# Optimization experiments

Measured on AMD Instinct MI355X. Metric: run time of the kernel, lower is better.

Reference implementation:

```python
import jax, jax.numpy as jnp
import numpy as np

B, T, E, H = 4, 2048, 512, 8
D = E // H  # head_dim = 64


def setup_inputs() -> dict:
    key = jax.random.key(0)
    ks = jax.random.split(key, 9)
    s = 1.0 / np.sqrt(E)
    inp = {
        "x": jax.random.normal(ks[0], (B, T, E), dtype=jnp.float32),
        "Wq": jax.random.normal(ks[1], (E, E), dtype=jnp.float32) * s,
        "bq": jnp.zeros((E,), dtype=jnp.float32),
        "Wk": jax.random.normal(ks[2], (E, E), dtype=jnp.float32) * s,
        "bk": jnp.zeros((E,), dtype=jnp.float32),
        "Wv": jax.random.normal(ks[3], (E, E), dtype=jnp.float32) * s,
        "bv": jnp.zeros((E,), dtype=jnp.float32),
        "Wo": jax.random.normal(ks[4], (E, E), dtype=jnp.float32) * s,
        "bo": jnp.zeros((E,), dtype=jnp.float32),
    }
    return inp


def reference(x, Wq, bq, Wk, bk, Wv, bv, Wo, bo):
    # x: (B, T, E); weights stored (in, out) so y = x @ W + b
    b, t, _ = x.shape
    q = (x @ Wq + bq).reshape(b, t, H, D).transpose(0, 2, 1, 3)  # (B,H,T,D)
    k = (x @ Wk + bk).reshape(b, t, H, D).transpose(0, 2, 1, 3)  # (B,H,T,D)
    v = (x @ Wv + bv).reshape(b, t, H, D).transpose(0, 2, 1, 3)  # (B,H,T,D)
    scores = jnp.einsum("bhqd,bhkd->bhqk", q, k) / np.sqrt(D)    # (B,H,Tq,Tk)
    # faithful to source: softmax over dim=-2 (the query axis)
    attn = jax.nn.softmax(scores, axis=-2)
    out = jnp.einsum("bhqk,bhkd->bhqd", attn, v)                  # (B,H,T,D)
    # faithful to source: reshape (B,H,T,D) -> (B,T,H*D) with NO transpose
    out = out.reshape(b, t, H * D)
    return out @ Wo + bo
```

## Files before the change

kernel.cpp:

```cpp
#include <hip/hip_runtime.h>
#include <hip/hip_bf16.h>

#define NB 4
#define NT 2048
#define NE 512
#define NH 8
#define ND 64
#define BH (NB*NH)

#define LOG2E 1.44269504088896340736f

typedef __attribute__((ext_vector_type(8))) short short8;
typedef __attribute__((ext_vector_type(4))) short short4v;
typedef __attribute__((ext_vector_type(4))) float f32x4;

typedef const __attribute__((address_space(3))) short* lds_sp;

__device__ __forceinline__ f32x4 mfma16(short8 a, short8 b, f32x4 c){
  return __builtin_amdgcn_mfma_f32_16x16x32_bf16(a, b, c, 0, 0, 0);
}
__device__ __forceinline__ short f2b(float f){
  union { float f; unsigned u; } v; v.f = f;
  unsigned r = v.u + 0x7FFFu + ((v.u >> 16) & 1u);
  return (short)(r >> 16);
}
__device__ __forceinline__ float b2f(short s){
  union { unsigned u; float f; } v; v.u = ((unsigned)(unsigned short)s) << 16; return v.f;
}
__device__ __forceinline__ unsigned pk2(float a, float b){
  union { __hip_bfloat162 h; unsigned u; } v;
  v.h = __float22bfloat162_rn(make_float2(a, b));
  return v.u;
}
__device__ __forceinline__ float fexp2(float x){
#if __has_builtin(__builtin_amdgcn_exp2f)
  return __builtin_amdgcn_exp2f(x);
#else
  return __expf(0.69314718055994530942f * x);
#endif
}
__device__ __forceinline__ void gld16(const void* g, void* l){
  __builtin_amdgcn_global_load_lds((const __attribute__((address_space(1))) void*)g,
                                   (__attribute__((address_space(3))) void*)l, 16, 0, 0);
}
__device__ __forceinline__ short4v trr(lds_sp p, int imm){
  short4v r;
  asm volatile("ds_read_b64_tr_b16 %0, %1 offset:%2" : "=v"(r) : "v"(p), "i"(imm));
  return r;
}

__global__ __launch_bounds__(256) void pack_all_k(const float* __restrict__ x, short* __restrict__ xb,
                                                  const float* __restrict__ Wq, const float* __restrict__ Wk,
                                                  const float* __restrict__ Wv, const float* __restrict__ Wo,
                                                  short* __restrict__ Wt){
  int bid = blockIdx.x;
  if (bid < 2048){
    int i = bid*256 + threadIdx.x;
    f32x4 a = ((const f32x4*)x)[2*i];
    f32x4 b = ((const f32x4*)x)[2*i+1];
    union { short8 s; unsigned u[4]; } o;
    o.u[0] = pk2(a[0], a[1]);
    o.u[1] = pk2(a[2], a[3]);
    o.u[2] = pk2(b[0], b[1]);
    o.u[3] = pk2(b[2], b[3]);
    ((short8*)xb)[i] = o.s;
  } else {
    int wb = bid - 2048;
    int z = wb >> 8;
    int rem = wb & 255;
    int j0 = (rem & 15)*32, e0 = (rem >> 4)*32;
    const float* W = z==0?Wq: z==1?Wk: z==2?Wv:Wo;
    short* out = Wt + (size_t)z*NE*NE;
    __shared__ float t[32][33];
    int tx = threadIdx.x & 31, ty = threadIdx.x >> 5;
#pragma unroll
    for (int r = 0; r < 4; ++r)
      t[ty*4+r][tx] = W[(size_t)(e0+ty*4+r)*NE + j0+tx];
    __syncthreads();
#pragma unroll
    for (int r = 0; r < 4; ++r)
      out[(size_t)(j0+ty*4+r)*NE + e0+tx] = f2b(t[tx][ty*4+r]);
  }
}

__global__ __launch_bounds__(256) void gemm_qkv_k(const short* __restrict__ xb, const short* __restrict__ Wt,
                                                  const float* __restrict__ bq, const float* __restrict__ bk,
                                                  const float* __restrict__ bv,
                                                  short* __restrict__ Q, short* __restrict__ K, short* __restrict__ V){
  int bid = blockIdx.x;
  int xcd = bid & 7;
  int j = bid >> 3;
  int n0 = (j & 3) * 128;
  int p = xcd*24 + (j >> 2);
  int z = p >> 6;
  int m0 = (p & 63) * 128;

  const short* Bm = Wt + (size_t)z*NE*NE;
  const float* bias = z==0?bq: z==1?bk:bv;
  short* out = z==0?Q: z==1?K:V;
  float scale = (z==0) ? 0.125f*LOG2E : 1.0f;

  __shared__ short As[128*64];
  __shared__ short Bs[128*64];
  int tid = threadIdx.x, lane = tid & 63, wid = tid >> 6;
  int wm = wid >> 1, wn = wid & 1;
  int sr = lane >> 3, sg = lane & 7;
  int fr = lane & 15, fg = lane >> 4;

  f32x4 acc[4][4] = {};

  for (int kt = 0; kt < 8; ++kt){
    int k0 = kt*64;
#pragma unroll
    for (int jj = 0; jj < 4; ++jj){
      int ii = wid*4 + jj;
      int r = ii*8 + sr;
      gld16(xb + (size_t)(m0 + r)*NE + k0 + ((sg ^ sr)<<3), (short*)As + ii*512);
      gld16(Bm + (size_t)(n0 + r)*NE + k0 + ((sg ^ sr)<<3), (short*)Bs + ii*512);
    }
    __syncthreads();
    short8 af[4][2], bf[4][2];
#pragma unroll
    for (int m = 0; m < 4; ++m){
      int row = wm*64 + m*16 + fr;
#pragma unroll
      for (int dh = 0; dh < 2; ++dh)
        af[m][dh] = *(const short8*)&As[row*64 + (((dh*4+fg) ^ (row&7))<<3)];
    }
#pragma unroll
    for (int n = 0; n < 4; ++n){
      int row = wn*64 + n*16 + fr;
#pragma unroll
      for (int dh = 0; dh < 2; ++dh)
        bf[n][dh] = *(const short8*)&Bs[row*64 + (((dh*4+fg) ^ (row&7))<<3)];
    }
#pragma unroll
    for (int m = 0; m < 4; ++m)
#pragma unroll
      for (int n = 0; n < 4; ++n){
        acc[m][n] = mfma16(af[m][0], bf[n][0], acc[m][n]);
        acc[m][n] = mfma16(af[m][1], bf[n][1], acc[m][n]);
      }
    __syncthreads();
  }
#pragma unroll
  for (int m = 0; m < 4; ++m)
#pragma unroll
    for (int n = 0; n < 4; ++n)
#pragma unroll
      for (int i = 0; i < 4; ++i){
        int row = m0 + wm*64 + m*16 + fg*4 + i;
        int col = n0 + wn*64 + n*16 + fr;
        float v = (acc[m][n][i] + bias[col]) * scale;
        int b = row >> 11, t = row & (NT-1), h = col >> 6, d = col & 63;
        out[(((size_t)(b*NH + h)*NT + t)<<6) + d] = f2b(v);
      }
}

__global__ __launch_bounds__(512, 4) void attn_l_k(const short* __restrict__ Q, const short* __restrict__ K,
                                                   const short* __restrict__ V, short* __restrict__ Vp){
  int bid = blockIdx.x;
  int bh = (bid & 7)*4 + ((bid >> 3) & 3);
  int kt = bid >> 5;
  const short* Qh = Q + (size_t)bh*NT*ND;
  const short* Kh = K + (size_t)bh*NT*ND;
  __shared__ short Qs0[8192];
  __shared__ short Qs1[8192];
  __shared__ float rl_all[128];
  int tid = threadIdx.x, lane = tid&63, wid = tid>>6;
  int fr = lane&15, fg = lane>>4;
  int sr = lane>>3, sg = lane&7;

  int krow = kt*128 + wid*16;
  short8 ak[2];
#pragma unroll
  for (int dh = 0; dh < 2; ++dh)
    ak[dh] = *(const short8*)&Kh[(size_t)(krow + fr)*ND + dh*32 + fg*8];

  const short* qsrc0 = Qh + (size_t)(wid*16 + sr)*ND + ((sg ^ sr)<<3);
  const short* qsrc1 = qsrc0 + 8*ND;
  auto stageQ = [&](short* qb, int t){
    size_t adv = (size_t)t*128*ND;
    gld16(qsrc0 + adv, qb + wid*1024);
    gld16(qsrc1 + adv, qb + wid*1024 + 512);
  };

  float rs[4] = {0.f,0.f,0.f,0.f};

  auto computeQ = [&](const short* Qt){
#pragma unroll
    for (int qf = 0; qf < 8; ++qf){
      int row = qf*16 + fr;
      short8 b0 = *(const short8*)&Qt[row*64 + ((fg ^ (row&7))<<3)];
      short8 b1 = *(const short8*)&Qt[row*64 + (((4+fg) ^ (row&7))<<3)];
      f32x4 c = {};
      c = mfma16(ak[0], b0, c);
      c = mfma16(ak[1], b1, c);
#pragma unroll
      for (int i = 0; i < 4; ++i)
        rs[i] += fexp2(c[i]);
    }
  };

  stageQ(Qs0, 0);
  __syncthreads();

  for (int qt2 = 0; qt2 < 8; ++qt2){
    int qtA = qt2*2;
    stageQ(Qs1, qtA+1);
    computeQ(Qs0);
    __syncthreads();
    if (qtA+2 < 16) stageQ(Qs0, qtA+2);
    computeQ(Qs1);
    __syncthreads();
  }

#pragma unroll
  for (int i = 0; i < 4; ++i){
    float v = rs[i];
    v += __shfl_xor(v, 1); v += __shfl_xor(v, 2);
    v += __shfl_xor(v, 4); v += __shfl_xor(v, 8);
    if (fr == 0) rl_all[wid*16 + fg*4 + i] = 1.0f / v;
  }
  {
    int row = tid >> 2;
    int col0 = (tid & 3) * 16;
    float inv = rl_all[row];
    const short* vsrc = V  + (size_t)bh*NT*ND + (size_t)(kt*128 + row)*ND + col0;
    short*       vdst = Vp + (size_t)bh*NT*ND + (size_t)(kt*128 + row)*ND + col0;
    short8 v0 = *(const short8*)vsrc;
    short8 v1 = *(const short8*)(vsrc + 8);
    union { short8 s; unsigned u[4]; } o0, o1;
#pragma unroll
    for (int j = 0; j < 4; ++j){
      o0.u[j] = pk2(b2f(v0[2*j])*inv, b2f(v0[2*j+1])*inv);
      o1.u[j] = pk2(b2f(v1[2*j])*inv, b2f(v1[2*j+1])*inv);
    }
    *(short8*)vdst       = o0.s;
    *(short8*)(vdst + 8) = o1.s;
  }
}

__global__ __launch_bounds__(256, 3) void attn_out_k(const short* __restrict__ Q, const short* __restrict__ K,
                                                     const short* __restrict__ Vp,
                                                     short* __restrict__ out2){
  int bid = blockIdx.x;
  int xcd = bid & 7, w = bid >> 3;
  int bh = xcd*4 + (w & 3);
  int q0 = (w >> 2) * 128;
  int b = bh >> 3, h = bh & 7;
  const short* Qh = Q + (size_t)bh*NT*ND;
  const short* Kh = K + (size_t)bh*NT*ND;
  const short* Vh = Vp + (size_t)bh*NT*ND;
  __shared__ short S0[8192];
  __shared__ short S1[8192];
  int tid = threadIdx.x, lane = tid&63, wid = tid>>6;
  int fr = lane&15, fg = lane>>4;
  int sr = lane>>3, sg = lane&7;
  int qw = q0 + wid*32;

  short8 qreg[2][2];
#pragma unroll
  for (int qf = 0; qf < 2; ++qf)
#pragma unroll
    for (int dh = 0; dh < 2; ++dh)
      qreg[qf][dh] = *(const short8*)&Qh[(size_t)(qw + qf*16 + fr)*ND + dh*32 + fg*8];

  const short* ksrc0 = Kh + (size_t)(wid*16 + sr)*ND + ((sg ^ sr)<<3);
  const short* ksrc1 = ksrc0 + 8*ND;
  int vt0 = wid*4 + (lane>>5);
  int vt1 = vt0 + 2;
  int vr = (lane&31)>>1, vc0 = (lane&1)*8;
  const short* vsrc0 = Vh + (size_t)((vt0>>2)*16 + vr)*ND + (vt0&3)*16 + vc0;
  const short* vsrc1 = Vh + (size_t)((vt1>>2)*16 + vr)*ND + (vt1&3)*16 + vc0;

  auto stage2 = [&](short* sb, int t){
    size_t adv = (size_t)t*64*ND;
    gld16(ksrc0 + adv, sb + wid*1024);
    gld16(ksrc1 + adv, sb + wid*1024 + 512);
    gld16(vsrc0 + adv, sb + 4096 + wid*1024);
    gld16(vsrc1 + adv, sb + 4096 + wid*1024 + 512);
  };

  f32x4 oacc[2][4] = {};

  auto compute = [&](const short* Ks, const short* Vs){
    short8 ak[4][2];
#pragma unroll
    for (int rf = 0; rf < 4; ++rf){
      int row = rf*16 + fr;
#pragma unroll
      for (int dh = 0; dh < 2; ++dh)
        ak[rf][dh] = *(const short8*)&Ks[row*64 + (((dh*4+fg) ^ (row&7))<<3)];
    }
    short8 pa[2][2];
#pragma unroll
    for (int qf = 0; qf < 2; ++qf){
      f32x4 s[4];
      __builtin_amdgcn_s_setprio(1);
#pragma unroll
      for (int rf = 0; rf < 4; ++rf){
        f32x4 c = {};
        c = mfma16(ak[rf][0], qreg[qf][0], c);
        c = mfma16(ak[rf][1], qreg[qf][1], c);
        s[rf] = c;
      }
      __builtin_amdgcn_s_setprio(0);
#pragma unroll
      for (int c = 0; c < 2; ++c){
        union { short8 s8; unsigned u[4]; } p;
        p.u[0] = pk2(fexp2(s[2*c  ][0]), fexp2(s[2*c  ][1]));
        p.u[1] = pk2(fexp2(s[2*c  ][2]), fexp2(s[2*c  ][3]));
        p.u[2] = pk2(fexp2(s[2*c+1][0]), fexp2(s[2*c+1][1]));
        p.u[3] = pk2(fexp2(s[2*c+1][2]), fexp2(s[2*c+1][3]));
        pa[qf][c] = p.s8;
      }
    }

    lds_sp vbase = (lds_sp)(Vs + lane*4);
#pragma unroll
    for (int c = 0; c < 2; ++c){
      short4v t0[4], t1[4];
#pragma unroll
      for (int n = 0; n < 4; ++n){
        t0[n] = trr(vbase, ((2*c  )*4 + n)*512);
        t1[n] = trr(vbase, ((2*c+1)*4 + n)*512);
      }
      asm volatile("s_waitcnt lgkmcnt(0)");
      __builtin_amdgcn_sched_barrier(0);
      __builtin_amdgcn_s_setprio(1);
#pragma unroll
      for (int n = 0; n < 4; ++n){
        short8 vb = __builtin_shufflevector(t0[n], t1[n], 0,1,2,3,4,5,6,7);
#pragma unroll
        for (int qf = 0; qf < 2; ++qf)
          oacc[qf][n] = mfma16(pa[qf][c], vb, oacc[qf][n]);
      }
      __builtin_amdgcn_s_setprio(0);
    }
  };

  stage2(S0, 0);
  __syncthreads();

  for (int kt2 = 0; kt2 < 16; ++kt2){
    int ktA = kt2*2;
    stage2(S1, ktA+1);
    compute(S0, S0 + 4096);
    __syncthreads();
    if (ktA+2 < 32) stage2(S0, ktA+2);
    compute(S1, S1 + 4096);
    __syncthreads();
  }

#pragma unroll
  for (int qf = 0; qf < 2; ++qf)
#pragma unroll
    for (int n = 0; n < 4; ++n)
#pragma unroll
      for (int i = 0; i < 4; ++i){
        int t = qw + qf*16 + fg*4 + i;
        int d = n*16 + fr;
        int r = h*256 + (t>>3);
        int e = ((t&7)<<6) + d;
        out2[((size_t)(b*NT + r)<<9) + e] = f2b(oacc[qf][n][i]);
      }
}

__global__ __launch_bounds__(256) void gemm_out_k(const short* __restrict__ A, const short* __restrict__ Bm,
                                                  const float* __restrict__ bo, float* __restrict__ out){
  int bid = blockIdx.x;
  int xcd = bid & 7;
  int j = bid >> 3;
  int n0 = (j & 3) * 128;
  int m0 = (xcd*8 + (j >> 2)) * 128;

  __shared__ short As[128*64];
  __shared__ short Bs[128*64];
  int tid = threadIdx.x, lane = tid & 63, wid = tid >> 6;
  int wm = wid >> 1, wn = wid & 1;
  int sr = lane >> 3, sg = lane & 7;
  int fr = lane & 15, fg = lane >> 4;

  f32x4 acc[4][4] = {};

  for (int kt = 0; kt < 8; ++kt){
    int k0 = kt*64;
#pragma unroll
    for (int jj = 0; jj < 4; ++jj){
      int ii = wid*4 + jj;
      int r = ii*8 + sr;
      gld16(A  + (size_t)(m0 + r)*NE + k0 + ((sg ^ sr)<<3), (short*)As + ii*512);
      gld16(Bm + (size_t)(n0 + r)*NE + k0 + ((sg ^ sr)<<3), (short*)Bs + ii*512);
    }
    __syncthreads();
    short8 af[4][2], bf[4][2];
#pragma unroll
    for (int m = 0; m < 4; ++m){
      int row = wm*64 + m*16 + fr;
#pragma unroll
      for (int dh = 0; dh < 2; ++dh)
        af[m][dh] = *(const short8*)&As[row*64 + (((dh*4+fg) ^ (row&7))<<3)];
    }
#pragma unroll
    for (int n = 0; n < 4; ++n){
      int row = wn*64 + n*16 + fr;
#pragma unroll
      for (int dh = 0; dh < 2; ++dh)
        bf[n][dh] = *(const short8*)&Bs[row*64 + (((dh*4+fg) ^ (row&7))<<3)];
    }
#pragma unroll
    for (int m = 0; m < 4; ++m)
#pragma unroll
      for (int n = 0; n < 4; ++n){
        acc[m][n] = mfma16(af[m][0], bf[n][0], acc[m][n]);
        acc[m][n] = mfma16(af[m][1], bf[n][1], acc[m][n]);
      }
    __syncthreads();
  }
#pragma unroll
  for (int m = 0; m < 4; ++m)
#pragma unroll
    for (int n = 0; n < 4; ++n)
#pragma unroll
      for (int i = 0; i < 4; ++i){
        int row = m0 + wm*64 + m*16 + fg*4 + i;
        int col = n0 + wn*64 + n*16 + fr;
        out[(size_t)row*NE + col] = acc[m][n][i] + bo[col];
      }
}

extern "C" void kernel_launch(void* const* d_in, const int* in_sizes, int n_in,
                              void* d_out, int out_size, void* d_ws, size_t ws_size,
                              hipStream_t stream){
  const float* x  = (const float*)d_in[0];
  const float* Wq = (const float*)d_in[1];
  const float* bq = (const float*)d_in[2];
  const float* Wk = (const float*)d_in[3];
  const float* bk = (const float*)d_in[4];
  const float* Wv = (const float*)d_in[5];
  const float* bv = (const float*)d_in[6];
  const float* Wo = (const float*)d_in[7];
  const float* bo = (const float*)d_in[8];
  float* out = (float*)d_out;

  char* ws = (char*)d_ws;
  size_t off = 0;
  auto alloc = [&](size_t bytes){ void* p = ws + off; off = (off + bytes + 255) & ~(size_t)255; return p; };
  short* xb    = (short*)alloc((size_t)NB*NT*NE*2);
  short* Wt    = (short*)alloc((size_t)4*NE*NE*2);
  short* Qb    = (short*)alloc((size_t)NB*NT*NE*2);
  short* Kb    = (short*)alloc((size_t)NB*NT*NE*2);
  short* Vb    = (short*)alloc((size_t)NB*NT*NE*2);
  short* Vp    = (short*)alloc((size_t)NB*NT*NE*2);
  short* out2  = (short*)alloc((size_t)NB*NT*NE*2);
  (void)ws_size; (void)in_sizes; (void)n_in; (void)out_size;

  pack_all_k<<<dim3(2048 + 1024), dim3(256), 0, stream>>>(x, xb, Wq, Wk, Wv, Wo, Wt);
  gemm_qkv_k<<<dim3(768), dim3(256), 0, stream>>>(xb, Wt, bq, bk, bv, Qb, Kb, Vb);
  attn_l_k<<<dim3((NT/128)*BH), dim3(512), 0, stream>>>(Qb, Kb, Vb, Vp);
  attn_out_k<<<dim3((NT/128)*BH), dim3(256), 0, stream>>>(Qb, Kb, Vp, out2);
  gemm_out_k<<<dim3(256), dim3(256), 0, stream>>>(out2, Wt + (size_t)3*NE*NE, bo, out);
}
```

Before: 104.4 us.

## Triple-buffer Q/K-V staging in attention kernels with one barrier per stage

Both attention kernels move from double-buffered LDS tiles with two full __syncthreads per pair to a three-buffer ring. Each stage now uses one barrier, preceded by a partial s_waitcnt vmcnt wait, so the next tile's global-to-LDS loads stay in flight while the current tile is computed. The aim is to cut barrier and load-latency stalls. The cost is an extra 16 KB of LDS per block, which may lower the number of resident blocks for the attn_l kernel (launch bounds 512,4). The hand-counted vmcnt values depend on how many loads each stage issues.

```diff
diff --git a/kernel.cpp b/kernel.cpp
--- a/kernel.cpp
+++ b/kernel.cpp
@@ -47,6 +47,16 @@
   short4v r;
   asm volatile("ds_read_b64_tr_b16 %0, %1 offset:%2" : "=v"(r) : "v"(p), "i"(imm));
   return r;
+}
+__device__ __forceinline__ void cbar4(){
+  asm volatile("s_waitcnt vmcnt(4)" ::: "memory");
+  __builtin_amdgcn_s_barrier();
+  __builtin_amdgcn_sched_barrier(0);
+}
+__device__ __forceinline__ void cbar0(){
+  asm volatile("s_waitcnt vmcnt(0)" ::: "memory");
+  __builtin_amdgcn_s_barrier();
+  __builtin_amdgcn_sched_barrier(0);
 }
 
 __global__ __launch_bounds__(256) void pack_all_k(const float* __restrict__ x, short* __restrict__ xb,
@@ -166,6 +176,7 @@
   const short* Kh = K + (size_t)bh*NT*ND;
   __shared__ short Qs0[8192];
   __shared__ short Qs1[8192];
+  __shared__ short Qs2[8192];
   __shared__ float rl_all[128];
   int tid = threadIdx.x, lane = tid&63, wid = tid>>6;
   int fr = lane&15, fg = lane>>4;
@@ -203,17 +214,26 @@
   };
 
   stageQ(Qs0, 0);
-  __syncthreads();
-
-  for (int qt2 = 0; qt2 < 8; ++qt2){
-    int qtA = qt2*2;
-    stageQ(Qs1, qtA+1);
+  stageQ(Qs1, 1);
+
+  for (int j5 = 0; j5 < 5; ++j5){
+    int t = j5*3;
+    asm volatile("s_waitcnt vmcnt(2)" ::: "memory");
+    __builtin_amdgcn_s_barrier(); __builtin_amdgcn_sched_barrier(0);
+    if (t+2 <= 15) stageQ(Qs2, t+2);
     computeQ(Qs0);
-    __syncthreads();
-    if (qtA+2 < 16) stageQ(Qs0, qtA+2);
+    asm volatile("s_waitcnt vmcnt(2)" ::: "memory");
+    __builtin_amdgcn_s_barrier(); __builtin_amdgcn_sched_barrier(0);
+    if (t+3 <= 15) stageQ(Qs0, t+3);
     computeQ(Qs1);
-    __syncthreads();
-  }
+    asm volatile("s_waitcnt vmcnt(2)" ::: "memory");
+    __builtin_amdgcn_s_barrier(); __builtin_amdgcn_sched_barrier(0);
+    if (t+4 <= 15) stageQ(Qs1, t+4);
+    computeQ(Qs2);
+  }
+  asm volatile("s_waitcnt vmcnt(0)" ::: "memory");
+  __builtin_amdgcn_s_barrier(); __builtin_amdgcn_sched_barrier(0);
+  computeQ(Qs0);
 
 #pragma unroll
   for (int i = 0; i < 4; ++i){
@@ -254,6 +274,7 @@
   const short* Vh = Vp + (size_t)bh*NT*ND;
   __shared__ short S0[8192];
   __shared__ short S1[8192];
+  __shared__ short S2[8192];
   int tid = threadIdx.x, lane = tid&63, wid = tid>>6;
   int fr = lane&15, fg = lane>>4;
   int sr = lane>>3, sg = lane&7;
@@ -341,17 +362,16 @@
   };
 
   stage2(S0, 0);
-  __syncthreads();
-
-  for (int kt2 = 0; kt2 < 16; ++kt2){
-    int ktA = kt2*2;
-    stage2(S1, ktA+1);
-    compute(S0, S0 + 4096);
-    __syncthreads();
-    if (ktA+2 < 32) stage2(S0, ktA+2);
-    compute(S1, S1 + 4096);
-    __syncthreads();
-  }
+  stage2(S1, 1);
+
+  for (int j3 = 0; j3 < 10; ++j3){
+    int t = j3*3;
+    cbar4(); stage2(S2, t+2); compute(S0, S0 + 4096);
+    cbar4(); stage2(S0, t+3); compute(S1, S1 + 4096);
+    cbar4(); stage2(S1, t+4); compute(S2, S2 + 4096);
+  }
+  cbar4(); compute(S0, S0 + 4096);
+  cbar0(); compute(S1, S1 + 4096);
 
 #pragma unroll
   for (int qf = 0; qf < 2; ++qf)
```

Measured after the change: 106.8 us. +2.3%, slower.
